# Kernel tuning notes

Measured on AMD Instinct MI355X. Metric: run time of the kernel, lower is better.

Reference implementation:

```python
import jax, jax.numpy as jnp
import numpy as np
from jax import lax

WS = 8  # window size

def conv1x1(x, W, b=None):
    y = jnp.einsum('bchw,oc->bohw', x, W)
    if b is not None:
        y = y + b[None, :, None, None]
    return y

def conv2d(x, W, b=None, dilation=1, groups=1):
    p = dilation * (W.shape[-1] // 2)
    y = lax.conv_general_dilated(x, W, (1, 1), [(p, p), (p, p)],
                                 rhs_dilation=(dilation, dilation),
                                 feature_group_count=groups,
                                 dimension_numbers=('NCHW', 'OIHW', 'NCHW'))
    if b is not None:
        y = y + b[None, :, None, None]
    return y

def ln_cf(x, w, b, eps=1e-6):
    # channels_first LayerNorm over channel dim
    u = x.mean(1, keepdims=True)
    s = ((x - u) ** 2).mean(1, keepdims=True)
    return w[None, :, None, None] * ((x - u) / jnp.sqrt(s + eps)) + b[None, :, None, None]

def to_windows(x):
    # b c (h dh) (w dw) -> b (h w) (dh dw c)
    B, C, H, W = x.shape
    h, w = H // WS, W // WS
    return x.reshape(B, C, h, WS, w, WS).transpose(0, 2, 4, 3, 5, 1).reshape(B, h * w, WS * WS * C)

def from_windows(x, C, H, W):
    B = x.shape[0]
    h, w = H // WS, W // WS
    return x.reshape(B, h, w, WS, WS, C).transpose(0, 5, 1, 3, 2, 4).reshape(B, C, H, W)

def lrelu(x):
    return jnp.where(x >= 0, x, 0.1 * x)

def gelu(x):
    return jax.nn.gelu(x, approximate=False)  # torch exact GELU

def _forward(x, w_norm1, b_norm1, w_norm2, b_norm2,
             Wv, bv, Wq, bq, Wk, bk, dw1, dwb1, dw2, dwb2, Wo, bo,
             W_in, b_in, Wc, bc, ln_w, ln_b, Wm1, bm1, Wm2, bm2,
             Wca, bca, Wsa, bsa, Wffn_in, dw_ffn, Wffn_out):
    B, C, H, W = x.shape
    ws2 = WS * WS
    N = (H // WS) * (W // WS)
    embed = ws2 * C
    # ---------- CAMixer ----------
    v = conv1x1(x, Wv, bv)
    # MaskPre routing
    xin = lrelu(conv1x1(v, W_in, b_in))                 # (B, C/4, H, W)
    x_ = lrelu(ln_cf(conv1x1(v, Wc, bc), ln_w, ln_b))   # (B, C/4, H, W)
    ca = jax.nn.sigmoid(conv1x1(x_.mean((2, 3), keepdims=True), Wca, bca))  # (B,C,1,1)
    sa = jax.nn.sigmoid(conv2d(x_, Wsa, bsa))           # (B,1,H,W)
    xm = to_windows(xin.mean(1, keepdims=True))         # (B,N,ws2)
    var = jnp.var(xm, axis=-1, ddof=1)                  # (B,N) torch.var unbiased
    k_top = N // 2
    _, idx = lax.top_k(-var, k_top)                     # bottom-k variance windows
    mbin = jnp.ones((B, N), x.dtype).at[jnp.arange(B)[:, None], idx].set(0.0)
    mfeat = jnp.broadcast_to(mbin[:, :, None], (B, N, embed))
    mask = lrelu(mfeat @ Wm1.T + bm1) @ Wm2.T + bm2     # (B,N,embed)
    # windowed content-routed attention
    vs = v * sa
    v_w, vs_w, x_w = to_windows(v), to_windows(vs), to_windows(x)
    v1 = (v_w * mask).reshape(B * N, ws2, C)
    v2 = vs_w * (1.0 - mask)
    t = (x_w * mask).reshape(B * N, ws2, C)             # masked q/k tokens (q=k=x)
    q1 = t @ Wq.T + bq
    k1 = t @ Wk.T + bk
    attn = jax.nn.softmax(q1 @ k1.transpose(0, 2, 1), axis=-1)  # (B*N, ws2, ws2)
    f = (attn @ v1).reshape(B, N, embed)
    img = from_windows(f + v2, C, H, W)
    cs = conv2d(conv2d(img, dw1, dwb1, 1, C), dw2, dwb2, 2, C)  # depthwise 3x3 + dilated
    out = gelu(cs) * ca + img
    res = conv1x1(out, Wo, bo)
    # ---------- norm1 + gated FFN + norm2 ----------
    x = ln_cf(x + res, w_norm1, b_norm1)
    y = conv2d(conv1x1(x, Wffn_in), dw_ffn, None, 1, 2 * C)
    y1, y2 = jnp.split(y, 2, axis=1)
    res = conv1x1(gelu(y1) * y2, Wffn_out)
    return ln_cf(x + res, w_norm2, b_norm2)

def setup_inputs():
    key = jax.random.key(0)
    B, C, H, W = 4, 64, 256, 256
    embed = WS * WS * C
    ks = iter(jax.random.split(key, 40))
    r = lambda *s: jax.random.normal(next(ks), s, jnp.float32) * 0.1
    return dict(
        x=jax.random.normal(next(ks), (B, C, H, W), jnp.float32),
        w_norm1=jnp.ones((C,), jnp.float32), b_norm1=jnp.zeros((C,), jnp.float32),
        w_norm2=jnp.ones((C,), jnp.float32), b_norm2=jnp.zeros((C,), jnp.float32),
        Wv=r(C, C), bv=r(C), Wq=r(C, C), bq=r(C), Wk=r(C, C), bk=r(C),
        dw1=r(C, 1, 3, 3), dwb1=r(C), dw2=r(C, 1, 3, 3), dwb2=r(C),
        Wo=r(C, C), bo=r(C),
        W_in=r(C // 4, C), b_in=r(C // 4), Wc=r(C // 4, C), bc=r(C // 4),
        ln_w=jnp.ones((C // 4,), jnp.float32), ln_b=jnp.zeros((C // 4,), jnp.float32),
        Wm1=r(embed // 2, embed) * 0.2, bm1=r(embed // 2),
        Wm2=r(embed, embed // 2) * 0.2, bm2=r(embed),
        Wca=r(C, C // 4), bca=r(C), Wsa=r(1, C // 4, 3, 3), bsa=r(1),
        Wffn_in=r(2 * C, C), dw_ffn=r(2 * C, 1, 3, 3), Wffn_out=r(C, C),
    )

def reference(x, w_norm1, b_norm1, w_norm2, b_norm2,
              Wv, bv, Wq, bq, Wk, bk, dw1, dwb1, dw2, dwb2, Wo, bo,
              W_in, b_in, Wc, bc, ln_w, ln_b, Wm1, bm1, Wm2, bm2,
              Wca, bca, Wsa, bsa, Wffn_in, dw_ffn, Wffn_out):
    return _forward(x, w_norm1, b_norm1, w_norm2, b_norm2,
                    Wv, bv, Wq, bq, Wk, bk, dw1, dwb1, dw2, dwb2, Wo, bo,
                    W_in, b_in, Wc, bc, ln_w, ln_b, Wm1, bm1, Wm2, bm2,
                    Wca, bca, Wsa, bsa, Wffn_in, dw_ffn, Wffn_out)
```

## Files before the change

kernel.cpp:

```cpp
#include <hip/hip_runtime.h>
#include <hip/hip_bf16.h>

typedef __hip_bfloat16 bf16;
typedef __attribute__((ext_vector_type(8))) short short8v;
typedef __attribute__((ext_vector_type(4))) float f32x4;

#define DEV static __device__ __forceinline__

DEV float b2f(bf16 h){ return __bfloat162float(h); }
DEV float us2f(unsigned short u){ unsigned v=((unsigned)u)<<16; float f; __builtin_memcpy(&f,&v,4); return f; }
DEV short f2bs(float f){ bf16 h=__float2bfloat16(f); short s; __builtin_memcpy(&s,&h,2); return s; }
DEV unsigned pack2(float a, float b){ return ((unsigned)(unsigned short)f2bs(b)<<16)|(unsigned short)f2bs(a); }
DEV float lrelu(float x){ return x >= 0.f ? x : 0.1f*x; }
DEV float geluf(float x){ return 0.5f*x*(1.f + erff(x*0.70710678118654752440f)); }
DEV float sigmoidf(float x){ return 1.f/(1.f + expf(-x)); }


__global__ __launch_bounds__(256) void k_detect(const void* x, int* flag){
  __shared__ int cnt;
  if(threadIdx.x==0) cnt=0;
  __syncthreads();
  const unsigned short* up=(const unsigned short*)x;
  int c=0;
  for(int k=0;k<16;k++){
    unsigned short u=up[(threadIdx.x*16+k)*2];
    if(((u>>7)&0xFF)==0xFF) c++;
  }
  atomicAdd(&cnt,c);
  __syncthreads();
  if(threadIdx.x==0) flag[0] = (cnt>0) ? 1 : 0;
}

struct CvtArgs { const void* src[31]; int sz[31]; int off[31]; };
__global__ __launch_bounds__(256) void k_cvt(CvtArgs a, const int* fl, float* wbuf){
  int t=blockIdx.x; int n=a.sz[t]; const void* s=a.src[t]; float* d=wbuf+a.off[t];
  if(fl[0]){
    const float* sp=(const float*)s;
    for(int i=threadIdx.x;i<n;i+=256) d[i]=sp[i];
  } else {
    const bf16* sp=(const bf16*)s;
    for(int i=threadIdx.x;i<n;i+=256) d[i]=b2f(sp[i]);
  }
}

__global__ __launch_bounds__(256) void k_w2b6(const float* __restrict__ wo, const float* __restrict__ wfi,
    const float* __restrict__ wfo, const float* __restrict__ wv,
    short* __restrict__ Wob, short* __restrict__ Wfib, short* __restrict__ Wfob,
    short* __restrict__ Wvb){
  int i=blockIdx.x*256+threadIdx.x;
  if(i<4096){ Wob[i]=f2bs(wo[i]); Wfob[i]=f2bs(wfo[i]); Wvb[i]=f2bs(wv[i]); }
  if(i<8192) Wfib[i]=f2bs(wfi[i]);
}

__global__ __launch_bounds__(256) void k_qkcomp(const float* __restrict__ wq, const float* __restrict__ wk,
    const float* __restrict__ bq, const float* __restrict__ bk,
    short* __restrict__ MtB, float* __restrict__ cvec, float* __restrict__ cconst){
  int idx=blockIdx.x*256+threadIdx.x;
  if(idx<4096){
    int cp=idx>>6, c=idx&63;
    float s=0.f;
    for(int o=0;o<64;o++) s+=wq[o*64+c]*wk[o*64+cp];
    MtB[cp*64+c]=f2bs(s);
  }
  if(blockIdx.x==0){
    int t=threadIdx.x;
    if(t<64){
      float s=0.f;
      for(int o=0;o<64;o++) s+=bq[o]*wk[o*64+t];
      cvec[t]=s;
    } else if(t==64){
      float s=0.f;
      for(int o=0;o<64;o++) s+=bq[o]*bk[o];
      cconst[0]=s;
    }
  }
}

__global__ __launch_bounds__(256) void k_wcomp(const float* __restrict__ W_in, const float* __restrict__ b_in,
    const float* __restrict__ Wc, const float* __restrict__ bc,
    const float* __restrict__ Wv, const float* __restrict__ bv,
    float* __restrict__ Wa, float* __restrict__ ba,
    float* __restrict__ Wb2, float* __restrict__ bb2){
  int t=threadIdx.x;
  #pragma unroll
  for(int ii=0;ii<4;ii++){
    int idx=t+ii*256;
    int i=idx>>6, c=idx&63;
    float sa=0.f, sb=0.f;
    for(int k=0;k<64;k++){
      float wv=Wv[k*64+c];
      sa+=W_in[i*64+k]*wv;
      sb+=Wc[i*64+k]*wv;
    }
    Wa[idx]=sa; Wb2[idx]=sb;
  }
  if(t<16){
    float sa=0.f, sb=0.f;
    for(int k=0;k<64;k++){ sa+=W_in[t*64+k]*bv[k]; sb+=Wc[t*64+k]*bv[k]; }
    ba[t]=sa+b_in[t]; bb2[t]=sb+bc[t];
  }
}

__global__ __launch_bounds__(256) void k_convv_mf(
    const void* __restrict__ in, const int* __restrict__ fl,
    const short* __restrict__ Wvb, const float* __restrict__ bv,
    const float* __restrict__ mbin, const float* __restrict__ m0T, const float* __restrict__ m1T,
    unsigned short* __restrict__ vw, unsigned short* __restrict__ xwb){
  __shared__ float Xf[64*66];
  int tid=threadIdx.x;
  int g0=blockIdx.x*64; int b=g0>>16, p0=g0&65535;
  int c=tid>>2, q=tid&3;
  size_t base=(((size_t)(b*64+c))<<16) + p0;
  if(fl[0]){
    const float* ip=(const float*)in + base;
    #pragma unroll
    for(int j=0;j<4;j++){
      int po=q*16+j*4;
      float4 xv=*(const float4*)(ip+po);
      *(float2*)&Xf[c*66+po]=make_float2(xv.x,xv.y);
      *(float2*)&Xf[c*66+po+2]=make_float2(xv.z,xv.w);
    }
  } else {
    const unsigned short* ip=(const unsigned short*)in + base;
    #pragma unroll
    for(int j=0;j<4;j++){
      int po=q*16+j*4;
      uint2 u=*(const uint2*)(ip+po);
      *(float2*)&Xf[c*66+po]=make_float2(us2f(u.x&0xffff),us2f(u.x>>16));
      *(float2*)&Xf[c*66+po+2]=make_float2(us2f(u.y&0xffff),us2f(u.y>>16));
    }
  }
  __syncthreads();
  int lane=tid&63, wid=tid>>6;
  int lr=lane&15, lg=lane>>4;
  int pix0=wid*16;
  short8v bfrag[2];
  #pragma unroll
  for(int ks=0;ks<2;ks++){
    short8v v;
    #pragma unroll
    for(int i=0;i<8;i++) v[i]=f2bs(Xf[(ks*32+lg*8+i)*66 + pix0+lr]);
    bfrag[ks]=v;
  }
  int y=p0>>8;
  int xx=(p0&255)+pix0+lr;
  int n=((y>>3)<<5)|(xx>>3), tok=((y&7)<<3)|(xx&7);
  unsigned short* wp=vw + (((size_t)(b*1024+n))<<12) + tok;
  #pragma unroll
  for(int nt=0;nt<4;nt++){
    f32x4 acc;
    #pragma unroll
    for(int r=0;r<4;r++) acc[r]=bv[nt*16+lg*4+r];
    #pragma unroll
    for(int ks=0;ks<2;ks++){
      short8v afrag=*(const short8v*)(Wvb + (nt*16+lr)*64 + ks*32 + lg*8);
      acc=__builtin_amdgcn_mfma_f32_16x16x32_bf16(afrag,bfrag[ks],acc,0,0,0);
    }
    #pragma unroll
    for(int r=0;r<4;r++){
      int m=nt*16+lg*4+r;
      wp[(size_t)m*64]=(unsigned short)f2bs(acc[r]);
    }
  }
  int nw0=((y>>3)<<5) | ((p0&255)>>3);
  int trow=(y&7)*8;
  #pragma unroll
  for(int k2=0;k2<2;k2++){
    int task=tid+k2*256;
    int w=task>>6, rem=task&63, j=rem>>3, cg=rem&7;
    int nn=nw0+w;
    const float* mT=(mbin[b*1024+nn]>0.5f)? m1T : m0T;
    int tk=trow+j;
    int pixl=w*8+j;
    unsigned short ov[8];
    #pragma unroll
    for(int i=0;i<8;i++){
      int ch=cg*8+i;
      ov[i]=(unsigned short)f2bs(Xf[ch*66+pixl]*mT[ch*64+tk]);
    }
    uint4 o;
    o.x=((unsigned)ov[1]<<16)|ov[0]; o.y=((unsigned)ov[3]<<16)|ov[2];
    o.z=((unsigned)ov[5]<<16)|ov[4]; o.w=((unsigned)ov[7]<<16)|ov[6];
    *(uint4*)(xwb + (((size_t)(b*1024+nn))<<12) + tk*64 + cg*8)=o;
  }
}

__global__ __launch_bounds__(256) void k_gemm_mf(
    const void* __restrict__ in, int in_f32,
    const short* __restrict__ Wb, const float* __restrict__ bias, int has_bias,
    void* __restrict__ out, int och, int out_bf16){
  __shared__ short Ain[64*72];
  int tid=threadIdx.x;
  int g0=blockIdx.x*64; int b=g0>>16, p0=g0&65535;
  int c=tid>>2, q=tid&3;
  size_t base=(((size_t)(b*64+c))<<16) + p0;
  if(in_f32){
    const float* ip=(const float*)in + base;
    #pragma unroll
    for(int j=0;j<4;j++){
      int po=q*16+j*4;
      float4 xv=*(const float4*)(ip+po);
      Ain[(po+0)*72+c]=f2bs(xv.x); Ain[(po+1)*72+c]=f2bs(xv.y);
      Ain[(po+2)*72+c]=f2bs(xv.z); Ain[(po+3)*72+c]=f2bs(xv.w);
    }
  } else {
    const unsigned short* ip=(const unsigned short*)in + base;
    #pragma unroll
    for(int j=0;j<4;j++){
      int po=q*16+j*4;
      uint2 u=*(const uint2*)(ip+po);
      Ain[(po+0)*72+c]=(short)(u.x&0xffff); Ain[(po+1)*72+c]=(short)(u.x>>16);
      Ain[(po+2)*72+c]=(short)(u.y&0xffff); Ain[(po+3)*72+c]=(short)(u.y>>16);
    }
  }
  __syncthreads();
  int lane=tid&63, wid=tid>>6;
  int lr=lane&15, lg=lane>>4;
  int pix0=wid*16;
  short8v bfrag[2];
  #pragma unroll
  for(int ks=0;ks<2;ks++) bfrag[ks]=*(const short8v*)&Ain[(pix0+lr)*72 + ks*32 + lg*8];
  int ntn=och>>4;
  for(int nt=0;nt<ntn;nt++){
    f32x4 acc;
    if(has_bias){
      #pragma unroll
      for(int r=0;r<4;r++) acc[r]=bias[nt*16+lg*4+r];
    } else {
      acc=(f32x4){0.f,0.f,0.f,0.f};
    }
    #pragma unroll
    for(int ks=0;ks<2;ks++){
      short8v afrag=*(const short8v*)(Wb + (nt*16+lr)*64 + ks*32 + lg*8);
      acc=__builtin_amdgcn_mfma_f32_16x16x32_bf16(afrag,bfrag[ks],acc,0,0,0);
    }
    if(out_bf16){
      unsigned short* op=(unsigned short*)out;
      #pragma unroll
      for(int r=0;r<4;r++){
        int m=nt*16+lg*4+r;
        op[(((size_t)(b*och+m))<<16) + p0 + pix0 + lr]=(unsigned short)f2bs(acc[r]);
      }
    } else {
      float* op=(float*)out;
      #pragma unroll
      for(int r=0;r<4;r++){
        int m=nt*16+lg*4+r;
        op[(((size_t)(b*och+m))<<16) + p0 + pix0 + lr]=acc[r];
      }
    }
  }
}

__global__ __launch_bounds__(256) void k_gemm_ln(
    const unsigned short* __restrict__ in,
    const short* __restrict__ Wb, const float* __restrict__ bias, int has_bias,
    const void* __restrict__ basex,
    const float* __restrict__ lnw, const float* __restrict__ lnb,
    void* __restrict__ out,
    const int* __restrict__ fl, int base_mode, int out_mode){
  __shared__ short Ain[64*72];
  int tid=threadIdx.x;
  int g0=blockIdx.x*64; int b=g0>>16, p0=g0&65535;
  int c=tid>>2, q=tid&3;
  {
    const unsigned short* ip=in + (((size_t)(b*64+c))<<16) + p0;
    #pragma unroll
    for(int j=0;j<4;j++){
      int po=q*16+j*4;
      uint2 u=*(const uint2*)(ip+po);
      Ain[(po+0)*72+c]=(short)(u.x&0xffff); Ain[(po+1)*72+c]=(short)(u.x>>16);
      Ain[(po+2)*72+c]=(short)(u.y&0xffff); Ain[(po+3)*72+c]=(short)(u.y>>16);
    }
  }
  __syncthreads();
  int lane=tid&63, wid=tid>>6;
  int lr=lane&15, lg=lane>>4;
  int pix0=wid*16;
  short8v bfrag[2];
  #pragma unroll
  for(int ks=0;ks<2;ks++) bfrag[ks]=*(const short8v*)&Ain[(pix0+lr)*72 + ks*32 + lg*8];
  float rl[16];
  #pragma unroll
  for(int nt=0;nt<4;nt++){
    f32x4 acc;
    if(has_bias){
      #pragma unroll
      for(int r=0;r<4;r++) acc[r]=bias[nt*16+lg*4+r];
    } else {
      acc=(f32x4){0.f,0.f,0.f,0.f};
    }
    #pragma unroll
    for(int ks=0;ks<2;ks++){
      short8v afrag=*(const short8v*)(Wb + (nt*16+lr)*64 + ks*32 + lg*8);
      acc=__builtin_amdgcn_mfma_f32_16x16x32_bf16(afrag,bfrag[ks],acc,0,0,0);
    }
    #pragma unroll
    for(int r=0;r<4;r++) rl[nt*4+r]=acc[r];
  }
  int pix=p0+pix0+lr;
  bool bf32 = (base_mode==1) || (base_mode==0 && fl[0]);
  if(bf32){
    const float* xp=(const float*)basex;
    #pragma unroll
    for(int nt=0;nt<4;nt++)
      #pragma unroll
      for(int r=0;r<4;r++)
        rl[nt*4+r]+=xp[(((size_t)(b*64+nt*16+lg*4+r))<<16)+pix];
  } else {
    const unsigned short* xp=(const unsigned short*)basex;
    #pragma unroll
    for(int nt=0;nt<4;nt++)
      #pragma unroll
      for(int r=0;r<4;r++)
        rl[nt*4+r]+=us2f(xp[(((size_t)(b*64+nt*16+lg*4+r))<<16)+pix]);
  }
  float s=0.f;
  #pragma unroll
  for(int i=0;i<16;i++) s+=rl[i];
  s+=__shfl_xor(s,16); s+=__shfl_xor(s,32);
  float mean=s*(1.f/64.f);
  float qv=0.f;
  #pragma unroll
  for(int i=0;i<16;i++){ float d=rl[i]-mean; qv+=d*d; }
  qv+=__shfl_xor(qv,16); qv+=__shfl_xor(qv,32);
  float inv=1.f/sqrtf(qv*(1.f/64.f)+1e-6f);
  bool of32 = (out_mode==1) || (out_mode==0 && fl[0]);
  if(of32){
    float* op=(float*)out;
    #pragma unroll
    for(int nt=0;nt<4;nt++)
      #pragma unroll
      for(int r=0;r<4;r++){
        int m=nt*16+lg*4+r;
        op[(((size_t)(b*64+m))<<16)+pix]=lnw[m]*((rl[nt*4+r]-mean)*inv)+lnb[m];
      }
  } else {
    unsigned short* op=(unsigned short*)out;
    #pragma unroll
    for(int nt=0;nt<4;nt++)
      #pragma unroll
      for(int r=0;r<4;r++){
        int m=nt*16+lg*4+r;
        op[(((size_t)(b*64+m))<<16)+pix]=(unsigned short)f2bs(lnw[m]*((rl[nt*4+r]-mean)*inv)+lnb[m]);
      }
  }
}

__global__ __launch_bounds__(256) void k_route(const void* __restrict__ x, const int* __restrict__ fl,
    const float* __restrict__ Wa, const float* __restrict__ ba,
    const float* __restrict__ Wb2, const float* __restrict__ bb2,
    const float* __restrict__ lnw, const float* __restrict__ lnb,
    float* __restrict__ x_, float* __restrict__ xm, float* __restrict__ capart){
  __shared__ float wA[1024], wB[1024], sba[16], sbb[16], slw[16], slb[16];
  __shared__ float sred[4][16];
  int tid=threadIdx.x;
  for(int i=tid;i<1024;i+=256){ wA[i]=Wa[i]; wB[i]=Wb2[i]; }
  if(tid<16){ sba[tid]=ba[tid]; sbb[tid]=bb2[tid]; slw[tid]=lnw[tid]; slb[tid]=lnb[tid]; }
  __syncthreads();
  int g=blockIdx.x*512+tid*2; int b=g>>16, p=g&65535;
  float2 aA[16], aB[16];
  #pragma unroll
  for(int i=0;i<16;i++){ aA[i]=make_float2(sba[i],sba[i]); aB[i]=make_float2(sbb[i],sbb[i]); }
  size_t base=(((size_t)b*64)<<16)+p;
  if(fl[0]){
    const float* vp=(const float*)x+base;
    for(int c=0;c<64;c++){
      float2 vv=*(const float2*)(vp+(((size_t)c)<<16));
      #pragma unroll
      for(int i=0;i<16;i++){
        float wa=wA[(i<<6)+c], wb=wB[(i<<6)+c];
        aA[i].x+=wa*vv.x; aA[i].y+=wa*vv.y;
        aB[i].x+=wb*vv.x; aB[i].y+=wb*vv.y;
      }
    }
  } else {
    const unsigned short* vp=(const unsigned short*)x+base;
    for(int c=0;c<64;c++){
      unsigned u=*(const unsigned*)(vp+(((size_t)c)<<16));
      float v0=us2f(u&0xffff), v1=us2f(u>>16);
      #pragma unroll
      for(int i=0;i<16;i++){
        float wa=wA[(i<<6)+c], wb=wB[(i<<6)+c];
        aA[i].x+=wa*v0; aA[i].y+=wa*v1;
        aB[i].x+=wb*v0; aB[i].y+=wb*v1;
      }
    }
  }
  float s0=0.f,s1=0.f;
  #pragma unroll
  for(int i=0;i<16;i++){ aA[i].x=lrelu(aA[i].x); aA[i].y=lrelu(aA[i].y); s0+=aA[i].x; s1+=aA[i].y; }
  float2 xmst; xmst.x=s0*(1.f/16.f); xmst.y=s1*(1.f/16.f);
  *(float2*)(xm+g)=xmst;
  float u0=0.f,u1=0.f;
  #pragma unroll
  for(int i=0;i<16;i++){ u0+=aB[i].x; u1+=aB[i].y; }
  u0*=(1.f/16.f); u1*=(1.f/16.f);
  float q0=0.f,q1=0.f;
  #pragma unroll
  for(int i=0;i<16;i++){ float d0=aB[i].x-u0, d1=aB[i].y-u1; q0+=d0*d0; q1+=d1*d1; }
  q0*=(1.f/16.f); q1*=(1.f/16.f);
  float i0=1.f/sqrtf(q0+1e-6f), i1=1.f/sqrtf(q1+1e-6f);
  float red[16];
  float* xp=x_+(((size_t)b*16)<<16)+p;
  #pragma unroll
  for(int i=0;i<16;i++){
    float xv0=lrelu(slw[i]*((aB[i].x-u0)*i0)+slb[i]);
    float xv1=lrelu(slw[i]*((aB[i].y-u1)*i1)+slb[i]);
    float2 st; st.x=xv0; st.y=xv1;
    *(float2*)(xp+(((size_t)i)<<16))=st;
    red[i]=xv0+xv1;
  }
  int lane=tid&63, wid=tid>>6;
  #pragma unroll
  for(int i=0;i<16;i++){
    float val=red[i];
    for(int m=32;m>0;m>>=1) val+=__shfl_xor(val,m);
    if(lane==0) sred[wid][i]=val;
  }
  __syncthreads();
  if(tid<16) capart[blockIdx.x*16+tid]=sred[0][tid]+sred[1][tid]+sred[2][tid]+sred[3][tid];
}

__global__ __launch_bounds__(256) void k_sa(const float* __restrict__ x_,
    const float* __restrict__ Wsa, const float* __restrict__ bsa, unsigned short* __restrict__ sa_w){
  __shared__ float w[144]; __shared__ float bb;
  int tid=threadIdx.x;
  if(tid<144) w[tid]=Wsa[tid];
  if(tid==0) bb=bsa[0];
  __syncthreads();
  int pix=blockIdx.x*256+tid; int b=pix>>16, p=pix&65535;
  int y=p>>8, xx=p&255;
  float acc=bb;
  #pragma unroll
  for(int i=0;i<16;i++){
    const float* pl=x_+(((size_t)(b*16+i))<<16);
    #pragma unroll
    for(int ky=0;ky<3;ky++){
      int yy=y+ky-1;
      if((unsigned)yy<256u){
        #pragma unroll
        for(int kx=0;kx<3;kx++){
          int x2=xx+kx-1;
          if((unsigned)x2<256u) acc+=pl[(yy<<8)+x2]*w[i*9+ky*3+kx];
        }
      }
    }
  }
  int n=((y>>3)<<5)|(xx>>3), tok=((y&7)<<3)|(xx&7);
  sa_w[(((size_t)(b<<10)+n)<<6)+tok]=(unsigned short)f2bs(sigmoidf(acc));
}

__global__ __launch_bounds__(64) void k_var(const float* __restrict__ xm, float* __restrict__ var){
  int blk=blockIdx.x, tid=threadIdx.x;
  int b=blk>>10, n=blk&1023;
  int pix=((n>>5)<<11) + ((n&31)<<3) + ((tid>>3)<<8) + (tid&7);
  float val=xm[(b<<16)+pix];
  float s=val;
  for(int m=32;m>0;m>>=1) s+=__shfl_xor(s,m);
  float mean=s*(1.f/64.f);
  float d=val-mean; float q=d*d;
  for(int m=32;m>0;m>>=1) q+=__shfl_xor(q,m);
  if(tid==0) var[blk]=q*(1.f/63.f);
}

__global__ __launch_bounds__(256) void k_rank(const float* __restrict__ var, float* __restrict__ mbin){
  __shared__ float va[1024];
  int bid=blockIdx.x; int b=bid>>2, seg=bid&3;
  int tid=threadIdx.x;
  for(int i=tid;i<1024;i+=256) va[i]=var[(b<<10)+i];
  __syncthreads();
  int n=seg*256+tid;
  float vn=va[n]; int r=0;
  for(int m=0;m<1024;m++){ float vm=va[m]; r += (vm<vn) || (vm==vn && m<n); }
  mbin[(b<<10)+n] = (r<512)?0.f:1.f;
}

__global__ __launch_bounds__(64) void k_hvec(const void* __restrict__ Wm1, const float* __restrict__ bm1,
    float* __restrict__ h0, float* __restrict__ h1, const int* __restrict__ fl){
  int j=blockIdx.x, tid=threadIdx.x;
  float s=0.f;
  if(fl[0]){
    const float* row=(const float*)Wm1+((size_t)j<<12);
    for(int k=tid;k<4096;k+=64) s+=row[k];
  } else {
    const bf16* row=(const bf16*)Wm1+((size_t)j<<12);
    for(int k=tid;k<4096;k+=64) s+=b2f(row[k]);
  }
  for(int m=32;m>0;m>>=1) s+=__shfl_xor(s,m);
  if(tid==0){ float bb=bm1[j]; h0[j]=lrelu(bb); h1[j]=lrelu(bb+s); }
}

__global__ __launch_bounds__(64) void k_mask(const void* __restrict__ Wm2, const float* __restrict__ bm2,
    const float* __restrict__ h0, const float* __restrict__ h1,
    float* __restrict__ m0, float* __restrict__ m1,
    float* __restrict__ m0T, float* __restrict__ m1T, const int* __restrict__ fl){
  int e=blockIdx.x, tid=threadIdx.x;
  float p0=0.f,p1=0.f;
  if(fl[0]){
    const float* row=(const float*)Wm2+((size_t)e<<11);
    for(int j=tid;j<2048;j+=64){ float w=row[j]; p0+=w*h0[j]; p1+=w*h1[j]; }
  } else {
    const bf16* row=(const bf16*)Wm2+((size_t)e<<11);
    for(int j=tid;j<2048;j+=64){ float w=b2f(row[j]); p0+=w*h0[j]; p1+=w*h1[j]; }
  }
  for(int m=32;m>0;m>>=1){ p0+=__shfl_xor(p0,m); p1+=__shfl_xor(p1,m); }
  if(tid==0){
    float bb=bm2[e]; float v0=p0+bb, v1=p1+bb;
    m0[e]=v0; m1[e]=v1;
    int te=(e&63)*64+(e>>6);
    m0T[te]=v0; m1T[te]=v1;
  }
}

__global__ __launch_bounds__(64) void k_ca(const float* __restrict__ capart,
    const float* __restrict__ Wca, const float* __restrict__ bca, float* __restrict__ ca){
  __shared__ float m[16];
  int b=blockIdx.x, tid=threadIdx.x;
  if(tid<16){
    float s=0.f;
    for(int blk=0;blk<128;blk++) s+=capart[((b*128)+blk)*16+tid];
    m[tid]=s*(1.f/65536.f);
  }
  __syncthreads();
  float a=bca[tid];
  #pragma unroll
  for(int i=0;i<16;i++) a+=Wca[(tid<<4)+i]*m[i];
  ca[(b<<6)+tid]=sigmoidf(a);
}

#define STR 72
#define STRF 65
__global__ __launch_bounds__(256) void k_attn_mfma(
    const unsigned short* __restrict__ xwb, const unsigned short* __restrict__ vw,
    const unsigned short* __restrict__ sa_w, const float* __restrict__ mbin,
    const float* __restrict__ m0T, const float* __restrict__ m1T,
    const short* __restrict__ MtB, const float* __restrict__ cvec, const float* __restrict__ cconst,
    unsigned short* __restrict__ img){
  __shared__ __align__(16) char uf[16640];
  __shared__ short sV1[64*STR];
  __shared__ float ssa[64];
  __shared__ float scv[64];
  short* sU=(short*)uf;
  float* sF=(float*)uf;
  int tid=threadIdx.x, blk=blockIdx.x;
  int b=blk>>10, n=blk&1023;
  int base=((n>>5)<<11) + ((n&31)<<3);
  size_t plane=((size_t)b*64)<<16;
  const float* mT = (mbin[blk]>0.5f)? m1T : m0T;
  const unsigned short* xw=xwb+(size_t)blk*4096;
  const unsigned short* vw2=vw+(size_t)blk*4096;
  int lane=tid&63, wid=tid>>6;
  int pb=wid*16, lr=lane&15, lg=lane>>4;
  short8v ta[2];
  #pragma unroll
  for(int ks=0;ks<2;ks++) ta[ks]=*(const short8v*)(xw + (pb+lr)*64 + ks*32 + lg*8);
  if(tid<64) ssa[tid]=us2f(sa_w[((size_t)blk<<6)+tid]);
  {
    int tok=tid>>2, part=tid&3;
    float s=0.f;
    #pragma unroll
    for(int i=0;i<16;i++){
      int c=part*16+i;
      s+=us2f(xw[tok*64+c])*cvec[c];
    }
    s+=__shfl_xor(s,1); s+=__shfl_xor(s,2);
    if(part==0) scv[tok]=s+cconst[0];
  }
  for(int task=tid;task<512;task+=256){
    int c=task>>3, tok0=(task&7)*8;
    uint4 uv=*(const uint4*)(vw2 + c*64 + tok0);
    float4 ma=*(const float4*)(mT + c*64 + tok0);
    float4 mb=*(const float4*)(mT + c*64 + tok0 + 4);
    uint4 o;
    o.x=pack2(us2f(uv.x&0xffff)*ma.x, us2f(uv.x>>16)*ma.y);
    o.y=pack2(us2f(uv.y&0xffff)*ma.z, us2f(uv.y>>16)*ma.w);
    o.z=pack2(us2f(uv.z&0xffff)*mb.x, us2f(uv.z>>16)*mb.y);
    o.w=pack2(us2f(uv.w&0xffff)*mb.z, us2f(uv.w>>16)*mb.w);
    *(uint4*)&sV1[c*STR+tok0]=o;
  }
  #pragma unroll
  for(int nt=0;nt<4;nt++){
    f32x4 ua={0.f,0.f,0.f,0.f};
    #pragma unroll
    for(int ks=0;ks<2;ks++){
      short8v afrag=*(const short8v*)(MtB + (nt*16+lr)*64 + ks*32 + lg*8);
      ua=__builtin_amdgcn_mfma_f32_16x16x32_bf16(afrag,ta[ks],ua,0,0,0);
    }
    uint2 w; w.x=pack2(ua[0],ua[1]); w.y=pack2(ua[2],ua[3]);
    *(uint2*)&sU[(pb+lr)*STR + nt*16+lg*4]=w;
  }
  __syncthreads();
  short8v qa2[2];
  #pragma unroll
  for(int ks=0;ks<2;ks++) qa2[ks]=*(const short8v*)&sU[(pb+lr)*STR + ks*32 + lg*8];
  f32x4 sacc[4];
  #pragma unroll
  for(int nt=0;nt<4;nt++){
    f32x4 a={0.f,0.f,0.f,0.f};
    #pragma unroll
    for(int ks=0;ks<2;ks++){
      short8v kb=*(const short8v*)(xw + (nt*16+lr)*64 + ks*32 + lg*8);
      a=__builtin_amdgcn_mfma_f32_16x16x32_bf16(qa2[ks],kb,a,0,0,0);
    }
    float cj=scv[nt*16+lr];
    #pragma unroll
    for(int r=0;r<4;r++) a[r]+=cj;
    sacc[nt]=a;
  }
  f32x4 pa[4];
  #pragma unroll
  for(int r=0;r<4;r++){
    float mx=fmaxf(fmaxf(sacc[0][r],sacc[1][r]),fmaxf(sacc[2][r],sacc[3][r]));
    #pragma unroll
    for(int m=1;m<16;m<<=1) mx=fmaxf(mx,__shfl_xor(mx,m));
    float e0=__expf(sacc[0][r]-mx), e1=__expf(sacc[1][r]-mx);
    float e2=__expf(sacc[2][r]-mx), e3=__expf(sacc[3][r]-mx);
    float sum=e0+e1+e2+e3;
    #pragma unroll
    for(int m=1;m<16;m<<=1) sum+=__shfl_xor(sum,m);
    float inv=1.f/sum;
    pa[0][r]=e0*inv; pa[1][r]=e1*inv; pa[2][r]=e2*inv; pa[3][r]=e3*inv;
  }
  #pragma unroll
  for(int nt=0;nt<4;nt++){
    #pragma unroll
    for(int r=0;r<4;r++)
      sU[(pb+lg*4+r)*STR + nt*16+lr]=f2bs(pa[nt][r]);
  }
  short8v aa[2];
  #pragma unroll
  for(int ks=0;ks<2;ks++) aa[ks]=*(const short8v*)&sU[(pb+lr)*STR + ks*32 + lg*8];
  unsigned pvv[8]; float pm0[8], pm1[8];
  #pragma unroll
  for(int it=0;it<8;it++){
    int e2=tid+it*256;
    int cc=e2>>5, tp=e2&31; int tok=tp*2;
    pvv[it]=*(const unsigned*)(vw2 + cc*64 + tok);
    pm0[it]=mT[cc*64+tok]; pm1[it]=mT[cc*64+tok+1];
  }
  __syncthreads();
  #pragma unroll
  for(int nt=0;nt<4;nt++){
    f32x4 f={0.f,0.f,0.f,0.f};
    #pragma unroll
    for(int ks=0;ks<2;ks++){
      short8v vb=*(const short8v*)&sV1[(nt*16+lr)*STR + ks*32 + lg*8];
      f=__builtin_amdgcn_mfma_f32_16x16x32_bf16(aa[ks],vb,f,0,0,0);
    }
    #pragma unroll
    for(int r=0;r<4;r++) sF[(pb+lg*4+r)*STRF + nt*16+lr]=f[r];
  }
  __syncthreads();
  #pragma unroll
  for(int it=0;it<8;it++){
    int e2=tid+it*256;
    int cc=e2>>5, tp=e2&31; int tok=tp*2;
    float f0=sF[tok*STRF+cc], f1=sF[(tok+1)*STRF+cc];
    float vs0=us2f(pvv[it]&0xffff)*ssa[tok]*(1.f-pm0[it]);
    float vs1=us2f(pvv[it]>>16)*ssa[tok+1]*(1.f-pm1[it]);
    int pix=base+((tok>>3)<<8)+(tok&7);
    *(unsigned*)(img+plane+(((size_t)cc)<<16)+pix)=pack2(f0+vs0, f1+vs1);
  }
}

#define DWI 264
__global__ __launch_bounds__(256) void k_dwfuse(const unsigned short* __restrict__ img,
    const float* __restrict__ dw1w, const float* __restrict__ dwb1,
    const float* __restrict__ dw2w, const float* __restrict__ dwb2,
    const float* __restrict__ ca, unsigned short* __restrict__ outb){
  __shared__ float sImg[22*DWI];
  __shared__ float sTmp[20*DWI];
  __shared__ float k1[9], k2[9];
  __shared__ float bb1, bb2, cav;
  int bid=blockIdx.x; int b=bid>>10, c=(bid>>4)&63, sy=bid&15;
  int y0=sy*16;
  int tid=threadIdx.x;
  if(tid<9){ k1[tid]=dw1w[c*9+tid]; k2[tid]=dw2w[c*9+tid]; }
  if(tid==9)  bb1=dwb1[c];
  if(tid==10) bb2=dwb2[c];
  if(tid==11) cav=ca[b*64+c];
  const unsigned short* ip=img+(((size_t)(b*64+c))<<16);
  for(int task=tid;task<1452;task+=256){
    int r=task/66, j=task-r*66;
    int gy=y0-3+r, gx0=4*j-4;
    float4 v=make_float4(0.f,0.f,0.f,0.f);
    if((unsigned)gy<256u && j>=1 && j<=64){
      uint2 u=*(const uint2*)(ip+(gy<<8)+gx0);
      v.x=us2f(u.x&0xffff); v.y=us2f(u.x>>16); v.z=us2f(u.y&0xffff); v.w=us2f(u.y>>16);
    }
    *(float4*)&sImg[r*DWI+4*j]=v;
  }
  __syncthreads();
  for(int task=tid;task<1300;task+=256){
    int r=task/65, g=task-r*65;
    int ty=y0-2+r, tc0=4*g-2;
    float t[4]={bb1,bb1,bb1,bb1};
    #pragma unroll
    for(int dy=0;dy<3;dy++){
      float4 A0=*(const float4*)&sImg[(r+dy)*DWI+4*g];
      float4 A1=*(const float4*)&sImg[(r+dy)*DWI+4*g+4];
      float F[8]={A0.x,A0.y,A0.z,A0.w,A1.x,A1.y,A1.z,A1.w};
      #pragma unroll
      for(int dx=0;dx<3;dx++){
        float kk=k1[dy*3+dx];
        #pragma unroll
        for(int e=0;e<4;e++) t[e]+=F[1+e+dx]*kk;
      }
    }
    float4 res;
    bool rowok=((unsigned)ty<256u);
    #pragma unroll
    for(int e=0;e<4;e++){
      int tc=tc0+e;
      ((float*)&res)[e]= (rowok && (unsigned)tc<256u)? t[e] : 0.f;
    }
    *(float4*)&sTmp[r*DWI+4*g]=res;
  }
  __syncthreads();
  int q=tid&63, rr=tid>>6;
  unsigned short* op=outb+(((size_t)(b*64+c))<<16);
  #pragma unroll
  for(int l4=0;l4<4;l4++){
    int ly=rr*4+l4;
    float cs[4]={bb2,bb2,bb2,bb2};
    #pragma unroll
    for(int dy=0;dy<3;dy++){
      int r=ly+2*dy;
      float4 T0=*(const float4*)&sTmp[r*DWI+4*q];
      float4 T1=*(const float4*)&sTmp[r*DWI+4*q+4];
      float T[8]={T0.x,T0.y,T0.z,T0.w,T1.x,T1.y,T1.z,T1.w};
      #pragma unroll
      for(int dx=0;dx<3;dx++){
        float kk=k2[dy*3+dx];
        #pragma unroll
        for(int e=0;e<4;e++) cs[e]+=T[e+2*dx]*kk;
      }
    }
    float4 C=*(const float4*)&sImg[(ly+3)*DWI+4*q+4];
    float o0=geluf(cs[0])*cav+C.x;
    float o1=geluf(cs[1])*cav+C.y;
    float o2=geluf(cs[2])*cav+C.z;
    float o3=geluf(cs[3])*cav+C.w;
    uint2 u; u.x=pack2(o0,o1); u.y=pack2(o2,o3);
    *(uint2*)(op+((y0+ly)<<8)+4*q)=u;
  }
}

#define FEI 264
__global__ __launch_bounds__(256) void k_ffn_dw_t(const unsigned short* __restrict__ E,
    const float* __restrict__ dwf, unsigned short* __restrict__ g){
  __shared__ unsigned short sE1[18*FEI];
  __shared__ unsigned short sE2[18*FEI];
  __shared__ float k1[9], k2[9];
  int bid=blockIdx.x; int b=bid>>10, c=(bid>>4)&63, sy=bid&15;
  int y0=sy*16;
  int tid=threadIdx.x;
  if(tid<9){ k1[tid]=dwf[c*9+tid]; k2[tid]=dwf[(64+c)*9+tid]; }
  const unsigned short* p1=E+(((size_t)(b*128+c))<<16);
  const unsigned short* p2=E+(((size_t)(b*128+64+c))<<16);
  for(int task=tid;task<1188;task+=256){
    int r=task/66, j=task-r*66;
    int gy=y0-1+r, gx0=4*j-4;
    uint2 u1=make_uint2(0,0), u2=make_uint2(0,0);
    if((unsigned)gy<256u && j>=1 && j<=64){
      u1=*(const uint2*)(p1+(gy<<8)+gx0);
      u2=*(const uint2*)(p2+(gy<<8)+gx0);
    }
    *(uint2*)&sE1[r*FEI+4*j]=u1;
    *(uint2*)&sE2[r*FEI+4*j]=u2;
  }
  __syncthreads();
  int q=tid&63, rr=tid>>6;
  unsigned short* op=g+(((size_t)(b*64+c))<<16);
  #pragma unroll
  for(int l4=0;l4<4;l4++){
    int ly=rr*4+l4;
    float a1[4]={0.f,0.f,0.f,0.f}, a2[4]={0.f,0.f,0.f,0.f};
    #pragma unroll
    for(int dy=0;dy<3;dy++){
      int r=ly+dy;
      unsigned w0=*(const unsigned*)&sE1[r*FEI+4*q+2];
      uint2   w1=*(const uint2*)  &sE1[r*FEI+4*q+4];
      unsigned w2=*(const unsigned*)&sE1[r*FEI+4*q+8];
      float GA[6]={us2f(w0>>16),us2f(w1.x&0xffff),us2f(w1.x>>16),us2f(w1.y&0xffff),us2f(w1.y>>16),us2f(w2&0xffff)};
      unsigned v0=*(const unsigned*)&sE2[r*FEI+4*q+2];
      uint2   v1=*(const uint2*)  &sE2[r*FEI+4*q+4];
      unsigned v2=*(const unsigned*)&sE2[r*FEI+4*q+8];
      float GB[6]={us2f(v0>>16),us2f(v1.x&0xffff),us2f(v1.x>>16),us2f(v1.y&0xffff),us2f(v1.y>>16),us2f(v2&0xffff)};
      #pragma unroll
      for(int dx=0;dx<3;dx++){
        float ka=k1[dy*3+dx], kb=k2[dy*3+dx];
        #pragma unroll
        for(int e=0;e<4;e++){
          a1[e]+=GA[e+dx]*ka;
          a2[e]+=GB[e+dx]*kb;
        }
      }
    }
    float o0=geluf(a1[0])*a2[0];
    float o1=geluf(a1[1])*a2[1];
    float o2=geluf(a1[2])*a2[2];
    float o3=geluf(a1[3])*a2[3];
    uint2 u; u.x=pack2(o0,o1); u.y=pack2(o2,o3);
    *(uint2*)(op+((y0+ly)<<8)+4*q)=u;
  }
}

extern "C" void kernel_launch(void* const* d_in, const int* in_sizes, int n_in,
                              void* d_out, int out_size, void* d_ws, size_t ws_size,
                              hipStream_t stream){
  (void)in_sizes; (void)n_in; (void)out_size; (void)ws_size;
  const void* x  = d_in[0];
  const void* Wm1= d_in[23];
  const void* Wm2= d_in[25];

  char* ws=(char*)d_ws;
  unsigned short* E=(unsigned short*)(ws);
  unsigned short* img=(unsigned short*)(ws+67108864);
  unsigned short* x1b=(unsigned short*)(ws+67108864);
  unsigned short* xwb=(unsigned short*)(ws+134217728);
  unsigned short* outb=(unsigned short*)(ws+134217728);
  unsigned short* gbuf=(unsigned short*)(ws+134217728);
  unsigned short* vw =(unsigned short*)(ws+230686720);
  char* sm = ws+201326592;
  float* x_    =(float*)(sm);
  unsigned short* sa_w=(unsigned short*)(sm+16777216);
  float* xm    =(float*)(sm+17825792);
  float* var   =(float*)(sm+18874368);
  float* mbin  =(float*)(sm+18890752);
  float* h0    =(float*)(sm+18907136);
  float* h1    =(float*)(sm+18915328);
  float* m0    =(float*)(sm+18923520);
  float* m1    =(float*)(sm+18939904);
  float* capart=(float*)(sm+18956288);
  float* ca    =(float*)(sm+19021824);
  int*   flag  =(int*)  (sm+19022848);
  float* wbuf  =(float*)(sm+19023872);
  float* m0T   =(float*)(sm+19216384);
  float* m1T   =(float*)(sm+19232768);
  short* Wob   =(short*)(sm+19249152);
  short* Wfib  =(short*)(sm+19257344);
  short* Wfob  =(short*)(sm+19273728);
  short* Wvb   =(short*)(sm+19281920);
  float* WaC   =(float*)(sm+19290112);
  float* WbC   =(float*)(sm+19294208);
  float* baC   =(float*)(sm+19298304);
  float* bbC   =(float*)(sm+19298560);
  short* MtB   =(short*)(sm+19298816);
  float* cvecD =(float*)(sm+19307008);
  float* cconstD=(float*)(sm+19307264);

  static const int din_idx[31]={5,6,7,8,9,10,11,12,13,14,15,16,17,18,19,20,21,22,24,26,27,28,29,30,31,32,33,1,2,3,4};
  static const int szs[31]  ={4096,64,4096,64,4096,64,576,64,576,64,4096,64,1024,16,1024,16,16,16,2048,4096,1024,64,144,1,8192,1152,4096,64,64,64,64};
  CvtArgs ca_args;
  int off=0;
  int offs[31];
  for(int t=0;t<31;t++){
    ca_args.src[t]=d_in[din_idx[t]];
    ca_args.sz[t]=szs[t];
    ca_args.off[t]=off;
    offs[t]=off;
    off+=szs[t];
  }
  const float* Wv  =wbuf+offs[0];  const float* bv  =wbuf+offs[1];
  const float* Wq  =wbuf+offs[2];  const float* bq  =wbuf+offs[3];
  const float* Wk  =wbuf+offs[4];  const float* bk  =wbuf+offs[5];
  const float* dw1 =wbuf+offs[6];  const float* dwb1=wbuf+offs[7];
  const float* dw2 =wbuf+offs[8];  const float* dwb2=wbuf+offs[9];
  const float* Wo  =wbuf+offs[10]; const float* bo  =wbuf+offs[11];
  const float* W_in=wbuf+offs[12]; const float* b_in=wbuf+offs[13];
  const float* Wc  =wbuf+offs[14]; const float* bc  =wbuf+offs[15];
  const float* lnw =wbuf+offs[16]; const float* lnb =wbuf+offs[17];
  const float* bm1 =wbuf+offs[18]; const float* bm2 =wbuf+offs[19];
  const float* Wca =wbuf+offs[20]; const float* bca =wbuf+offs[21];
  const float* Wsa =wbuf+offs[22]; const float* bsa =wbuf+offs[23];
  const float* Wfi =wbuf+offs[24]; const float* dwf =wbuf+offs[25];
  const float* Wfo =wbuf+offs[26];
  const float* wn1 =wbuf+offs[27]; const float* bn1 =wbuf+offs[28];
  const float* wn2 =wbuf+offs[29]; const float* bn2 =wbuf+offs[30];

  hipLaunchKernelGGL(k_detect,   dim3(1),      dim3(256), 0, stream, x, flag);
  hipLaunchKernelGGL(k_cvt,      dim3(31),     dim3(256), 0, stream, ca_args, flag, wbuf);
  hipLaunchKernelGGL(k_w2b6,     dim3(32),     dim3(256), 0, stream, Wo, Wfi, Wfo, Wv, Wob, Wfib, Wfob, Wvb);
  hipLaunchKernelGGL(k_qkcomp,   dim3(16),     dim3(256), 0, stream, Wq, Wk, bq, bk, MtB, cvecD, cconstD);
  hipLaunchKernelGGL(k_wcomp,    dim3(1),      dim3(256), 0, stream, W_in, b_in, Wc, bc, Wv, bv, WaC, baC, WbC, bbC);
  hipLaunchKernelGGL(k_route,    dim3(512),    dim3(256), 0, stream, x, flag, WaC, baC, WbC, bbC, lnw, lnb, x_, xm, capart);
  hipLaunchKernelGGL(k_sa,       dim3(1024),   dim3(256), 0, stream, x_, Wsa, bsa, sa_w);
  hipLaunchKernelGGL(k_var,      dim3(4096),   dim3(64),  0, stream, xm, var);
  hipLaunchKernelGGL(k_rank,     dim3(16),     dim3(256), 0, stream, var, mbin);
  hipLaunchKernelGGL(k_hvec,     dim3(2048),   dim3(64),  0, stream, Wm1, bm1, h0, h1, flag);
  hipLaunchKernelGGL(k_mask,     dim3(4096),   dim3(64),  0, stream, Wm2, bm2, h0, h1, m0, m1, m0T, m1T, flag);
  hipLaunchKernelGGL(k_ca,       dim3(4),      dim3(64),  0, stream, capart, Wca, bca, ca);
  hipLaunchKernelGGL(k_convv_mf, dim3(4096),   dim3(256), 0, stream, x, flag, Wvb, bv, mbin, m0T, m1T, vw, xwb);
  hipLaunchKernelGGL(k_attn_mfma,dim3(4096),   dim3(256), 0, stream, xwb, vw, sa_w, mbin, m0T, m1T, MtB, cvecD, cconstD, img);
  hipLaunchKernelGGL(k_dwfuse,   dim3(4096),   dim3(256), 0, stream, img, dw1, dwb1, dw2, dwb2, ca, outb);
  hipLaunchKernelGGL(k_gemm_ln,  dim3(4096),   dim3(256), 0, stream, outb, Wob, bo, 1, x, wn1, bn1, (void*)x1b, flag, 0, 2);
  hipLaunchKernelGGL(k_gemm_mf,  dim3(4096),   dim3(256), 0, stream, (const void*)x1b, 0, Wfib, wbuf, 0, (void*)E, 128, 1);
  hipLaunchKernelGGL(k_ffn_dw_t, dim3(4096),   dim3(256), 0, stream, E, dwf, gbuf);
  hipLaunchKernelGGL(k_gemm_ln,  dim3(4096),   dim3(256), 0, stream, gbuf, Wfob, wbuf, 0, (const void*)x1b, wn2, bn2, d_out, flag, 2, 0);
}
```

Measured before the change: 489.4 us.

## Merge setup kernels and compute attention residual term in registers with vector stores

The dtype-detection kernel is folded into the weight-conversion kernel, where every block recomputes the flag locally. The three weight-precompute kernels are merged into one 49-block launch, removing several small launches. In the attention kernel, the value*sa*(1-mask) residual term is computed in registers during the initial V staging, dropping a second pass of global loads and the shared sa buffer. Output stores become 16-byte vectors of 8 tokens instead of 4-byte pairs, at the cost of extra live registers.

```diff
diff --git a/kernel.cpp b/kernel.cpp
--- a/kernel.cpp
+++ b/kernel.cpp
@@ -16,7 +16,8 @@
 DEV float sigmoidf(float x){ return 1.f/(1.f + expf(-x)); }
 
 
-__global__ __launch_bounds__(256) void k_detect(const void* x, int* flag){
+struct CvtArgs { const void* src[31]; int sz[31]; int off[31]; };
+__global__ __launch_bounds__(256) void k_cvt(CvtArgs a, const void* x, int* flag, float* wbuf){
   __shared__ int cnt;
   if(threadIdx.x==0) cnt=0;
   __syncthreads();
@@ -28,13 +29,10 @@
   }
   atomicAdd(&cnt,c);
   __syncthreads();
-  if(threadIdx.x==0) flag[0] = (cnt>0) ? 1 : 0;
-}
-
-struct CvtArgs { const void* src[31]; int sz[31]; int off[31]; };
-__global__ __launch_bounds__(256) void k_cvt(CvtArgs a, const int* fl, float* wbuf){
+  int isf32 = (cnt>0);
+  if(blockIdx.x==0 && threadIdx.x==0) flag[0]=isf32;
   int t=blockIdx.x; int n=a.sz[t]; const void* s=a.src[t]; float* d=wbuf+a.off[t];
-  if(fl[0]){
+  if(isf32){
     const float* sp=(const float*)s;
     for(int i=threadIdx.x;i<n;i+=256) d[i]=sp[i];
   } else {
@@ -43,61 +41,61 @@
   }
 }
 
-__global__ __launch_bounds__(256) void k_w2b6(const float* __restrict__ wo, const float* __restrict__ wfi,
+__global__ __launch_bounds__(256) void k_prep(
+    const float* __restrict__ wo, const float* __restrict__ wfi,
     const float* __restrict__ wfo, const float* __restrict__ wv,
+    const float* __restrict__ wq, const float* __restrict__ wk,
+    const float* __restrict__ bq, const float* __restrict__ bk,
+    const float* __restrict__ W_in, const float* __restrict__ b_in,
+    const float* __restrict__ Wc, const float* __restrict__ bc,
+    const float* __restrict__ bv,
     short* __restrict__ Wob, short* __restrict__ Wfib, short* __restrict__ Wfob,
-    short* __restrict__ Wvb){
-  int i=blockIdx.x*256+threadIdx.x;
-  if(i<4096){ Wob[i]=f2bs(wo[i]); Wfob[i]=f2bs(wfo[i]); Wvb[i]=f2bs(wv[i]); }
-  if(i<8192) Wfib[i]=f2bs(wfi[i]);
-}
-
-__global__ __launch_bounds__(256) void k_qkcomp(const float* __restrict__ wq, const float* __restrict__ wk,
-    const float* __restrict__ bq, const float* __restrict__ bk,
-    short* __restrict__ MtB, float* __restrict__ cvec, float* __restrict__ cconst){
-  int idx=blockIdx.x*256+threadIdx.x;
-  if(idx<4096){
-    int cp=idx>>6, c=idx&63;
-    float s=0.f;
-    for(int o=0;o<64;o++) s+=wq[o*64+c]*wk[o*64+cp];
-    MtB[cp*64+c]=f2bs(s);
-  }
-  if(blockIdx.x==0){
-    int t=threadIdx.x;
-    if(t<64){
-      float s=0.f;
-      for(int o=0;o<64;o++) s+=bq[o]*wk[o*64+t];
-      cvec[t]=s;
-    } else if(t==64){
-      float s=0.f;
-      for(int o=0;o<64;o++) s+=bq[o]*bk[o];
-      cconst[0]=s;
-    }
-  }
-}
-
-__global__ __launch_bounds__(256) void k_wcomp(const float* __restrict__ W_in, const float* __restrict__ b_in,
-    const float* __restrict__ Wc, const float* __restrict__ bc,
-    const float* __restrict__ Wv, const float* __restrict__ bv,
+    short* __restrict__ Wvb, short* __restrict__ MtB,
+    float* __restrict__ cvec, float* __restrict__ cconst,
     float* __restrict__ Wa, float* __restrict__ ba,
     float* __restrict__ Wb2, float* __restrict__ bb2){
-  int t=threadIdx.x;
-  #pragma unroll
-  for(int ii=0;ii<4;ii++){
-    int idx=t+ii*256;
-    int i=idx>>6, c=idx&63;
-    float sa=0.f, sb=0.f;
-    for(int k=0;k<64;k++){
-      float wv=Wv[k*64+c];
-      sa+=W_in[i*64+k]*wv;
-      sb+=Wc[i*64+k]*wv;
-    }
-    Wa[idx]=sa; Wb2[idx]=sb;
-  }
-  if(t<16){
-    float sa=0.f, sb=0.f;
-    for(int k=0;k<64;k++){ sa+=W_in[t*64+k]*bv[k]; sb+=Wc[t*64+k]*bv[k]; }
-    ba[t]=sa+b_in[t]; bb2[t]=sb+bc[t];
+  int bid=blockIdx.x, tid=threadIdx.x;
+  if(bid<32){
+    int i=bid*256+tid;
+    if(i<4096){ Wob[i]=f2bs(wo[i]); Wfob[i]=f2bs(wfo[i]); Wvb[i]=f2bs(wv[i]); }
+    if(i<8192) Wfib[i]=f2bs(wfi[i]);
+  } else if(bid<48){
+    int idx=(bid-32)*256+tid;
+    if(idx<4096){
+      int cp=idx>>6, c=idx&63;
+      float s=0.f;
+      for(int o=0;o<64;o++) s+=wq[o*64+c]*wk[o*64+cp];
+      MtB[cp*64+c]=f2bs(s);
+    }
+    if(bid==32){
+      if(tid<64){
+        float s=0.f;
+        for(int o=0;o<64;o++) s+=bq[o]*wk[o*64+tid];
+        cvec[tid]=s;
+      } else if(tid==64){
+        float s=0.f;
+        for(int o=0;o<64;o++) s+=bq[o]*bk[o];
+        cconst[0]=s;
+      }
+    }
+  } else {
+    #pragma unroll
+    for(int ii=0;ii<4;ii++){
+      int idx=tid+ii*256;
+      int i=idx>>6, c=idx&63;
+      float sa=0.f, sb=0.f;
+      for(int k=0;k<64;k++){
+        float wv2=wv[k*64+c];
+        sa+=W_in[i*64+k]*wv2;
+        sb+=Wc[i*64+k]*wv2;
+      }
+      Wa[idx]=sa; Wb2[idx]=sb;
+    }
+    if(tid<16){
+      float sa=0.f, sb=0.f;
+      for(int k=0;k<64;k++){ sa+=W_in[tid*64+k]*bv[k]; sb+=Wc[tid*64+k]*bv[k]; }
+      ba[tid]=sa+b_in[tid]; bb2[tid]=sb+bc[tid];
+    }
   }
 }
 
@@ -539,7 +537,6 @@
     unsigned short* __restrict__ img){
   __shared__ __align__(16) char uf[16640];
   __shared__ short sV1[64*STR];
-  __shared__ float ssa[64];
   __shared__ float scv[64];
   short* sU=(short*)uf;
   float* sF=(float*)uf;
@@ -555,7 +552,6 @@
   short8v ta[2];
   #pragma unroll
   for(int ks=0;ks<2;ks++) ta[ks]=*(const short8v*)(xw + (pb+lr)*64 + ks*32 + lg*8);
-  if(tid<64) ssa[tid]=us2f(sa_w[((size_t)blk<<6)+tid]);
   {
     int tok=tid>>2, part=tid&3;
     float s=0.f;
@@ -567,17 +563,33 @@
     s+=__shfl_xor(s,1); s+=__shfl_xor(s,2);
     if(part==0) scv[tok]=s+cconst[0];
   }
-  for(int task=tid;task<512;task+=256){
+  float vs[16];
+  #pragma unroll
+  for(int k2=0;k2<2;k2++){
+    int task=tid+k2*256;
     int c=task>>3, tok0=(task&7)*8;
     uint4 uv=*(const uint4*)(vw2 + c*64 + tok0);
     float4 ma=*(const float4*)(mT + c*64 + tok0);
     float4 mb=*(const float4*)(mT + c*64 + tok0 + 4);
+    uint4 sa4=*(const uint4*)(sa_w + ((size_t)blk<<6) + tok0);
+    float v0=us2f(uv.x&0xffff), v1=us2f(uv.x>>16);
+    float v2=us2f(uv.y&0xffff), v3=us2f(uv.y>>16);
+    float v4=us2f(uv.z&0xffff), v5=us2f(uv.z>>16);
+    float v6=us2f(uv.w&0xffff), v7=us2f(uv.w>>16);
     uint4 o;
-    o.x=pack2(us2f(uv.x&0xffff)*ma.x, us2f(uv.x>>16)*ma.y);
-    o.y=pack2(us2f(uv.y&0xffff)*ma.z, us2f(uv.y>>16)*ma.w);
-    o.z=pack2(us2f(uv.z&0xffff)*mb.x, us2f(uv.z>>16)*mb.y);
-    o.w=pack2(us2f(uv.w&0xffff)*mb.z, us2f(uv.w>>16)*mb.w);
+    o.x=pack2(v0*ma.x, v1*ma.y);
+    o.y=pack2(v2*ma.z, v3*ma.w);
+    o.z=pack2(v4*mb.x, v5*mb.y);
+    o.w=pack2(v6*mb.z, v7*mb.w);
     *(uint4*)&sV1[c*STR+tok0]=o;
+    vs[k2*8+0]=v0*us2f(sa4.x&0xffff)*(1.f-ma.x);
+    vs[k2*8+1]=v1*us2f(sa4.x>>16)  *(1.f-ma.y);
+    vs[k2*8+2]=v2*us2f(sa4.y&0xffff)*(1.f-ma.z);
+    vs[k2*8+3]=v3*us2f(sa4.y>>16)  *(1.f-ma.w);
+    vs[k2*8+4]=v4*us2f(sa4.z&0xffff)*(1.f-mb.x);
+    vs[k2*8+5]=v5*us2f(sa4.z>>16)  *(1.f-mb.y);
+    vs[k2*8+6]=v6*us2f(sa4.w&0xffff)*(1.f-mb.z);
+    vs[k2*8+7]=v7*us2f(sa4.w>>16)  *(1.f-mb.w);
   }
   #pragma unroll
   for(int nt=0;nt<4;nt++){
@@ -631,14 +643,6 @@
   short8v aa[2];
   #pragma unroll
   for(int ks=0;ks<2;ks++) aa[ks]=*(const short8v*)&sU[(pb+lr)*STR + ks*32 + lg*8];
-  unsigned pvv[8]; float pm0[8], pm1[8];
-  #pragma unroll
-  for(int it=0;it<8;it++){
-    int e2=tid+it*256;
-    int cc=e2>>5, tp=e2&31; int tok=tp*2;
-    pvv[it]=*(const unsigned*)(vw2 + cc*64 + tok);
-    pm0[it]=mT[cc*64+tok]; pm1[it]=mT[cc*64+tok+1];
-  }
   __syncthreads();
   #pragma unroll
   for(int nt=0;nt<4;nt++){
@@ -653,14 +657,20 @@
   }
   __syncthreads();
   #pragma unroll
-  for(int it=0;it<8;it++){
-    int e2=tid+it*256;
-    int cc=e2>>5, tp=e2&31; int tok=tp*2;
-    float f0=sF[tok*STRF+cc], f1=sF[(tok+1)*STRF+cc];
-    float vs0=us2f(pvv[it]&0xffff)*ssa[tok]*(1.f-pm0[it]);
-    float vs1=us2f(pvv[it]>>16)*ssa[tok+1]*(1.f-pm1[it]);
-    int pix=base+((tok>>3)<<8)+(tok&7);
-    *(unsigned*)(img+plane+(((size_t)cc)<<16)+pix)=pack2(f0+vs0, f1+vs1);
+  for(int k2=0;k2<2;k2++){
+    int task=tid+k2*256;
+    int c=task>>3, tok0=(task&7)*8;
+    unsigned short ov[8];
+    #pragma unroll
+    for(int j=0;j<8;j++){
+      float f=sF[(tok0+j)*STRF+c];
+      ov[j]=(unsigned short)f2bs(f+vs[k2*8+j]);
+    }
+    uint4 o;
+    o.x=((unsigned)ov[1]<<16)|ov[0]; o.y=((unsigned)ov[3]<<16)|ov[2];
+    o.z=((unsigned)ov[5]<<16)|ov[4]; o.w=((unsigned)ov[7]<<16)|ov[6];
+    int pix=base+((tok0>>3)<<8);
+    *(uint4*)(img+plane+(((size_t)c)<<16)+pix)=o;
   }
 }
 
@@ -880,11 +890,9 @@
   const float* wn1 =wbuf+offs[27]; const float* bn1 =wbuf+offs[28];
   const float* wn2 =wbuf+offs[29]; const float* bn2 =wbuf+offs[30];
 
-  hipLaunchKernelGGL(k_detect,   dim3(1),      dim3(256), 0, stream, x, flag);
-  hipLaunchKernelGGL(k_cvt,      dim3(31),     dim3(256), 0, stream, ca_args, flag, wbuf);
-  hipLaunchKernelGGL(k_w2b6,     dim3(32),     dim3(256), 0, stream, Wo, Wfi, Wfo, Wv, Wob, Wfib, Wfob, Wvb);
-  hipLaunchKernelGGL(k_qkcomp,   dim3(16),     dim3(256), 0, stream, Wq, Wk, bq, bk, MtB, cvecD, cconstD);
-  hipLaunchKernelGGL(k_wcomp,    dim3(1),      dim3(256), 0, stream, W_in, b_in, Wc, bc, Wv, bv, WaC, baC, WbC, bbC);
+  hipLaunchKernelGGL(k_cvt,      dim3(31),     dim3(256), 0, stream, ca_args, x, flag, wbuf);
+  hipLaunchKernelGGL(k_prep,     dim3(49),     dim3(256), 0, stream, Wo, Wfi, Wfo, Wv, Wq, Wk, bq, bk,
+                     W_in, b_in, Wc, bc, bv, Wob, Wfib, Wfob, Wvb, MtB, cvecD, cconstD, WaC, baC, WbC, bbC);
   hipLaunchKernelGGL(k_route,    dim3(512),    dim3(256), 0, stream, x, flag, WaC, baC, WbC, bbC, lnw, lnb, x_, xm, capart);
   hipLaunchKernelGGL(k_sa,       dim3(1024),   dim3(256), 0, stream, x_, Wsa, bsa, sa_w);
   hipLaunchKernelGGL(k_var,      dim3(4096),   dim3(64),  0, stream, xm, var);
```

Result: faster. 477.7 us (-2.4%).
